# Performance work log

Hardware: AMD Instinct MI355X
Metric: run time of the kernel (lower is better)

Reference implementation:

```python
import jax, jax.numpy as jnp
import numpy as np

H = 768
NH = 12
HD = H // NH


def setup_inputs() -> dict:
    key = jax.random.key(0)
    ks = jax.random.split(key, 12)
    B, S = 2, 2048
    s = 1.0 / np.sqrt(H)
    inp = {
        "hidden_states": jax.random.normal(ks[0], (B, S, H), dtype=jnp.float32),
        "attention_mask": jnp.ones((B, S), dtype=jnp.float32),
        "Wq": jax.random.normal(ks[1], (H, H), dtype=jnp.float32) * s,
        "bq": jnp.zeros((H,), dtype=jnp.float32),
        "Wk": jax.random.normal(ks[2], (H, H), dtype=jnp.float32) * s,
        "bk": jnp.zeros((H,), dtype=jnp.float32),
        "Wv": jax.random.normal(ks[3], (H, H), dtype=jnp.float32) * s,
        "bv": jnp.zeros((H,), dtype=jnp.float32),
        "Wo": jax.random.normal(ks[4], (H, H), dtype=jnp.float32) * s,
        "bo": jnp.zeros((H,), dtype=jnp.float32),
        "ln_gamma": jnp.ones((H,), dtype=jnp.float32),
        "ln_beta": jnp.zeros((H,), dtype=jnp.float32),
    }
    return inp


def _split_heads(x):
    # [B,S,H] -> [B,NH,S,HD]
    B, S, _ = x.shape
    return x.reshape(B, S, NH, HD).transpose(0, 2, 1, 3)


def reference(hidden_states, attention_mask, Wq, bq, Wk, bk, Wv, bv, Wo, bo, ln_gamma, ln_beta):
    x = hidden_states
    q = _split_heads(x @ Wq.T + bq)
    k = _split_heads(x @ Wk.T + bk)
    v = _split_heads(x @ Wv.T + bv)
    # scores: [B,NH,S,S]
    scores = jnp.einsum("bhqd,bhkd->bhqk", q, k) / jnp.sqrt(jnp.float32(HD))
    mask = (1.0 - attention_mask)[:, None, None, :] * -10000.0
    scores = scores + mask
    probs = jax.nn.softmax(scores, axis=-1)  # dropout is identity at inference
    ctx = jnp.einsum("bhqk,bhkd->bhqd", probs, v)
    B, _, S, _ = ctx.shape
    ctx = ctx.transpose(0, 2, 1, 3).reshape(B, S, H)
    out = ctx @ Wo.T + bo
    y = out + x
    mu = jnp.mean(y, axis=-1, keepdims=True)
    var = jnp.var(y, axis=-1, keepdims=True)
    y = (y - mu) / jnp.sqrt(var + 1e-5)
    return y * ln_gamma + ln_beta
```

## Files before the change

kernel.cpp:

```cpp
#include <hip/hip_runtime.h>
#include <math.h>

#define HH 768
#define NHEADS 12
#define HDIM 64
#define SEQ 2048
#define NB 2
#define L2E 1.44269504088896f

typedef __attribute__((ext_vector_type(8))) short s8v;
typedef __attribute__((ext_vector_type(4))) short s4v;
typedef __attribute__((ext_vector_type(4))) float f4v;

static __device__ inline short f2bf(float f) {
    union { float f; unsigned u; } v; v.f = f;
    unsigned r = v.u + 0x7fff + ((v.u >> 16) & 1);
    return (short)(r >> 16);
}

#if __has_builtin(__builtin_amdgcn_exp2f)
#define EXP2(x) __builtin_amdgcn_exp2f(x)
#else
#define EXP2(x) __expf((x) * 0.6931471805599453f)
#endif

__device__ __forceinline__ unsigned cvt_pk_bf16(float a, float b) {
    unsigned r;
    asm("v_cvt_pk_bf16_f32 %0, %1, %2" : "=v"(r) : "v"(a), "v"(b));
    return r;
}

__device__ __forceinline__ void gld16(const void* g, void* l) {
    __builtin_amdgcn_global_load_lds(
        (const __attribute__((address_space(1))) void*)g,
        (__attribute__((address_space(3))) void*)l, 16, 0, 0);
}

__device__ __forceinline__ int kperm(int k) {
    return (k & ~31) | (((k >> 2) & 3) << 3) | (((k >> 4) & 1) << 2) | (k & 3);
}

#define XV8   393216
#define WV8   73728
__global__ __launch_bounds__(256)
void cvt_kernel(const float* __restrict__ X, short* __restrict__ Xb,
                const float* __restrict__ W0, short* __restrict__ W0b,
                const float* __restrict__ W1, short* __restrict__ W1b,
                const float* __restrict__ W2, short* __restrict__ W2b,
                const float* __restrict__ W3, short* __restrict__ W3b)
{
    int gid = blockIdx.x * 256 + threadIdx.x;
    const float* src; short* dst; size_t off;
    if      (gid < XV8)            { src = X;  dst = Xb;  off = gid; }
    else if (gid < XV8 + WV8)      { src = W0; dst = W0b; off = gid - XV8; }
    else if (gid < XV8 + 2*WV8)    { src = W1; dst = W1b; off = gid - XV8 - WV8; }
    else if (gid < XV8 + 3*WV8)    { src = W2; dst = W2b; off = gid - XV8 - 2*WV8; }
    else if (gid < XV8 + 4*WV8)    { src = W3; dst = W3b; off = gid - XV8 - 3*WV8; }
    else return;
    off *= 8;
    float4 a = *(const float4*)(src + off);
    float4 b = *(const float4*)(src + off + 4);
    s8v o;
    o[0] = f2bf(a.x); o[1] = f2bf(a.y); o[2] = f2bf(a.z); o[3] = f2bf(a.w);
    o[4] = f2bf(b.x); o[5] = f2bf(b.y); o[6] = f2bf(b.z); o[7] = f2bf(b.w);
    *(s8v*)(dst + off) = o;
}

#define NKT (HH/32)
template<int EPI>
__global__ __launch_bounds__(256)
void gemm_mfma(const short* __restrict__ A,
               const short* __restrict__ Wq, const short* __restrict__ Wk,
               const short* __restrict__ Wv,
               const float* __restrict__ bq, const float* __restrict__ bk,
               const float* __restrict__ bv,
               short* __restrict__ Qo, short* __restrict__ Ko, short* __restrict__ Vo,
               const float* __restrict__ Xres, float* __restrict__ Fo)
{
    __shared__ __align__(16) short As[2*64*32];
    __shared__ __align__(16) short Bs[2*128*32];

    const int tid  = threadIdx.x;
    const int w    = tid >> 6;
    const int lane = tid & 63;
    const int g    = lane >> 4;
    const int r    = lane & 15;
    const int wr   = w >> 1;
    const int wc   = w & 1;

    const int NI   = (EPI == 0) ? 4 : 2;
    const int BBUF = (EPI == 0) ? 4096 : 2048;

    const int NBX = (EPI == 0) ? 18 : 12;
    const int NXB = (EPI == 0) ? 144 : 96;
    const int wg  = (blockIdx.x & 7) * NXB + (blockIdx.x >> 3);
    const int bx  = wg % NBX;
    const int by  = wg / NBX;
    const int m0  = by * 64;

    int n0;
    int seg = 0;
    const short* Wb; const float* bias; short* outp; float scale;
    if (EPI == 0) {
        seg = bx / 6;
        n0 = (bx % 6) * 128;
        Wb   = seg == 0 ? Wq : seg == 1 ? Wk : Wv;
        bias = seg == 0 ? bq : seg == 1 ? bk : bv;
        outp = seg == 0 ? Qo : seg == 1 ? Ko : Vo;
        scale = seg == 0 ? (0.125f * L2E) : 1.0f;
    } else {
        n0 = bx * 64;
        Wb = Wq; bias = bq; outp = nullptr; scale = 1.0f;
    }

    const int uline = tid >> 3;
    const int us    = tid & 7;
    const int srow  = 2*uline + (us >> 2);
    const int scol  = 8 * ((us & 3) ^ (uline & 3));
    const short* Asrc  = A  + (size_t)(m0 + srow) * HH + scol;
    const short* Bsrc0 = Wb + (size_t)(n0 + srow) * HH + scol;
    const short* Bsrc1 = (EPI == 0) ? (Wb + (size_t)(n0 + 64 + srow) * HH + scol) : nullptr;

    #define GSTAGE(KT, DB) do { const int k0 = (KT) * 32;                      \
        gld16(Asrc  + k0, As + (DB)*2048 + w*512);                             \
        gld16(Bsrc0 + k0, Bs + (DB)*BBUF + w*512);                             \
        if (EPI == 0) gld16(Bsrc1 + k0, Bs + (DB)*BBUF + 2048 + w*512);        \
    } while (0)

    f4v acc[2][4];
    #pragma unroll
    for (int i = 0; i < 2; i++)
        #pragma unroll
        for (int j = 0; j < 4; j++) acc[i][j] = (f4v){0.f,0.f,0.f,0.f};

    const int keyg  = (g ^ ((r >> 1) & 3)) * 8;
    const int abase = (wr*16 + (r >> 1))*64 + (r & 1)*32 + keyg;
    const int wcl   = (EPI == 0) ? wc*32 : wc*16;
    const int bbase = (wcl + (r >> 1))*64 + (r & 1)*32 + keyg;

    #define GCOMPUTE(DB) do {                                                  \
        const short* Ab = As + (DB)*2048;                                      \
        const short* Bb = Bs + (DB)*BBUF;                                      \
        s8v af[2], bf[4];                                                      \
        _Pragma("unroll")                                                      \
        for (int mi = 0; mi < 2; mi++)                                         \
            af[mi] = *(const s8v*)(Ab + abase + mi*512);                       \
        _Pragma("unroll")                                                      \
        for (int ni = 0; ni < NI; ni++)                                        \
            bf[ni] = *(const s8v*)(Bb + bbase + ni*512);                       \
        __builtin_amdgcn_s_setprio(1);                                         \
        _Pragma("unroll")                                                      \
        for (int mi = 0; mi < 2; mi++)                                         \
            _Pragma("unroll")                                                  \
            for (int ni = 0; ni < NI; ni++)                                    \
                acc[mi][ni] = __builtin_amdgcn_mfma_f32_16x16x32_bf16(         \
                    af[mi], bf[ni], acc[mi][ni], 0, 0, 0);                     \
        __builtin_amdgcn_s_setprio(0);                                         \
    } while (0)

    GSTAGE(0, 0);

    for (int kt = 0; kt < NKT; ++kt) {
        if (kt + 1 < NKT) {
            GSTAGE(kt + 1, (kt + 1) & 1);
            if constexpr (EPI == 0) asm volatile("s_waitcnt vmcnt(3)" ::: "memory");
            else                    asm volatile("s_waitcnt vmcnt(2)" ::: "memory");
        } else {
            asm volatile("s_waitcnt vmcnt(0)" ::: "memory");
        }
        __builtin_amdgcn_s_barrier();
        GCOMPUTE(kt & 1);
        __builtin_amdgcn_s_barrier();
    }

    if (EPI == 0) {
        if (seg < 2) {
            #pragma unroll
            for (int mi = 0; mi < 2; mi++) {
                #pragma unroll
                for (int j = 0; j < 4; j++) {
                    const int m = m0 + wr*32 + mi*16 + 4*g + j;
                    const int bb = m >> 11;
                    const int s  = m & 2047;
                    #pragma unroll
                    for (int ni = 0; ni < 4; ni++) {
                        const int n = n0 + wc*64 + ni*16 + r;
                        const int h = n >> 6;
                        const int d = n & 63;
                        outp[((size_t)((bb*NHEADS + h)*SEQ) + s)*HDIM + d] =
                            f2bf((acc[mi][ni][j] + bias[n]) * scale);
                    }
                }
            }
        } else {
            #pragma unroll
            for (int mi = 0; mi < 2; mi++) {
                const int m  = m0 + wr*32 + mi*16 + 4*g;
                const int bb = m >> 11;
                const int s  = m & 2047;
                const int sp = kperm(s);
                #pragma unroll
                for (int ni = 0; ni < 4; ni++) {
                    const int n = n0 + wc*64 + ni*16 + r;
                    const int h = n >> 6;
                    const int d = n & 63;
                    s4v pk;
                    #pragma unroll
                    for (int j = 0; j < 4; j++)
                        pk[j] = f2bf(acc[mi][ni][j] + bias[n]);
                    *(s4v*)(outp + ((size_t)((bb*NHEADS + h)*HDIM) + d)*SEQ + sp) = pk;
                }
            }
        }
    } else {
        #pragma unroll
        for (int mi = 0; mi < 2; mi++) {
            #pragma unroll
            for (int j = 0; j < 4; j++) {
                const int m = m0 + wr*32 + mi*16 + 4*g + j;
                #pragma unroll
                for (int ni = 0; ni < 2; ni++) {
                    const int n = n0 + wc*32 + ni*16 + r;
                    Fo[(size_t)m*HH + n] = acc[mi][ni][j] + bias[n] + Xres[(size_t)m*HH + n];
                }
            }
        }
    }
    #undef GSTAGE
    #undef GCOMPUTE
}

#define NPAIR (SEQ/64)
__global__ __launch_bounds__(512, 4)
void attn_mfma(const short* __restrict__ Q, const short* __restrict__ K,
               const short* __restrict__ VT, const float* __restrict__ mask,
               short* __restrict__ CTX)
{
    const int wgid = (blockIdx.x & 7) * 96 + (blockIdx.x >> 3);
    const int qt = wgid & 31;
    const int bh = wgid >> 5;
    const int h  = bh % NHEADS;
    const int b  = bh / NHEADS;

    const size_t hb = (size_t)(b * NHEADS + h);
    const short* Qg  = Q  + hb * SEQ * HDIM;
    const short* Kg  = K  + hb * SEQ * HDIM;
    const short* VTg = VT + hb * HDIM * SEQ;

    __shared__ __align__(16) char lds[40960];
    char* Kbase = lds;
    char* Vbase = lds + 16384;
    float* Mf   = (float*)(lds + 32768);

    const int tid  = threadIdx.x;
    const int w    = tid >> 6;
    const int grp  = w >> 2;
    const int wq   = w & 3;
    const int lane = tid & 63;
    const int g    = lane >> 4;
    const int r    = lane & 15;
    const int q0   = qt * 64;

    const short* qrow = Qg + (size_t)(q0 + wq*16 + r) * HDIM;
    const s8v qf0 = *(const s8v*)(qrow + 8*g);
    const s8v qf1 = *(const s8v*)(qrow + 8*g + 32);

    {
        float4 mv = *(const float4*)(mask + b*SEQ + tid*4);
        f4v md;
        md[0] = (mv.x - 1.0f) * (10000.0f * L2E);
        md[1] = (mv.y - 1.0f) * (10000.0f * L2E);
        md[2] = (mv.z - 1.0f) * (10000.0f * L2E);
        md[3] = (mv.w - 1.0f) * (10000.0f * L2E);
        *(f4v*)(Mf + kperm(tid*4)) = md;
    }

    f4v acc[4];
    #pragma unroll
    for (int t = 0; t < 4; t++) acc[t] = (f4v){0.f, 0.f, 0.f, 0.f};
    f4v accl = (f4v){0.f, 0.f, 0.f, 0.f};
    const s8v ones = (s8v){0x3F80, 0x3F80, 0x3F80, 0x3F80,
                           0x3F80, 0x3F80, 0x3F80, 0x3F80};

    const int srow = lane >> 3;
    const int scol = 8 * ((lane & 7) ^ srow);

    #define STAGE(PT, DB) do {                                                 \
        const int pk0 = (PT) * 64;                                             \
        char* kd = Kbase + (DB)*8192 + w*1024;                                 \
        gld16(Kg + (size_t)(pk0 + 8*w + srow)*HDIM + scol, kd);                \
        char* vd = Vbase + (DB)*8192 + w*1024;                                 \
        gld16(VTg + (size_t)(8*w + srow)*SEQ + pk0 + scol, vd);                \
    } while (0)

    STAGE(0, 0);
    __syncthreads();

    for (int pt = 0; pt < NPAIR; ++pt) {
        const int db = pt & 1;
        if (pt + 1 < NPAIR) {
            STAGE(pt + 1, db ^ 1);
            asm volatile("s_waitcnt vmcnt(2)" ::: "memory");
        } else {
            asm volatile("s_waitcnt vmcnt(0)" ::: "memory");
        }
        __builtin_amdgcn_s_barrier();

        const char* Kc = Kbase + db*8192 + grp*4096;
        const char* Vc = Vbase + db*8192;

        const float* mrow = Mf + pt*64 + grp*32 + 8*g;
        f4v z0 = *(const f4v*)(mrow);
        f4v z1 = *(const f4v*)(mrow + 4);

        __builtin_amdgcn_s_setprio(1);
        {
            const int sw = (r & 7) << 4;
            const char* kb0 = Kc + r * 128;
            const char* kb1 = Kc + (16 + r) * 128;
            s8v ka0 = *(const s8v*)(kb0 + ((16*g)      ^ sw));
            s8v ka1 = *(const s8v*)(kb0 + ((16*g + 64) ^ sw));
            s8v kc0 = *(const s8v*)(kb1 + ((16*g)      ^ sw));
            s8v kc1 = *(const s8v*)(kb1 + ((16*g + 64) ^ sw));
            z0 = __builtin_amdgcn_mfma_f32_16x16x32_bf16(ka0, qf0, z0, 0, 0, 0);
            z0 = __builtin_amdgcn_mfma_f32_16x16x32_bf16(ka1, qf1, z0, 0, 0, 0);
            z1 = __builtin_amdgcn_mfma_f32_16x16x32_bf16(kc0, qf0, z1, 0, 0, 0);
            z1 = __builtin_amdgcn_mfma_f32_16x16x32_bf16(kc1, qf1, z1, 0, 0, 0);
        }
        __builtin_amdgcn_s_setprio(0);

        #pragma unroll
        for (int i = 0; i < 4; i++) {
            z0[i] = EXP2(z0[i]);
            z1[i] = EXP2(z1[i]);
        }

        union { unsigned u[4]; s8v v; } pfu;
        pfu.u[0] = cvt_pk_bf16(z0[0], z0[1]);
        pfu.u[1] = cvt_pk_bf16(z0[2], z0[3]);
        pfu.u[2] = cvt_pk_bf16(z1[0], z1[1]);
        pfu.u[3] = cvt_pk_bf16(z1[2], z1[3]);
        const s8v pf = pfu.v;

        accl = __builtin_amdgcn_mfma_f32_16x16x32_bf16(pf, ones, accl, 0, 0, 0);

        __builtin_amdgcn_s_setprio(1);
        #pragma unroll
        for (int t4 = 0; t4 < 4; t4++) {
            const int vrow = 16*t4 + r;
            s8v vf = *(const s8v*)(Vc + vrow*128 + ((16*(4*grp + g)) ^ ((r & 7) << 4)));
            acc[t4] = __builtin_amdgcn_mfma_f32_16x16x32_bf16(pf, vf, acc[t4], 0, 0, 0);
        }
        __builtin_amdgcn_s_setprio(0);

        __builtin_amdgcn_s_barrier();
    }

    __syncthreads();
    if (grp == 1) {
        float* mb = (float*)(lds + wq*5120 + lane*80);
        *(f4v*)(mb)      = acc[0];
        *(f4v*)(mb + 4)  = acc[1];
        *(f4v*)(mb + 8)  = acc[2];
        *(f4v*)(mb + 12) = acc[3];
        *(f4v*)(mb + 16) = accl;
    }
    __syncthreads();
    if (grp == 0) {
        const float* mb = (const float*)(lds + wq*5120 + lane*80);
        acc[0] += *(const f4v*)(mb);
        acc[1] += *(const f4v*)(mb + 4);
        acc[2] += *(const f4v*)(mb + 8);
        acc[3] += *(const f4v*)(mb + 12);
        accl   += *(const f4v*)(mb + 16);

        #pragma unroll
        for (int i = 0; i < 4; i++) {
            const float invl = 1.0f / accl[i];
            const size_t rowbase = ((size_t)(b*SEQ) + q0 + wq*16 + 4*g + i) * HH + h*HDIM;
            #pragma unroll
            for (int t4 = 0; t4 < 4; t4++)
                CTX[rowbase + 16*t4 + r] = f2bf(acc[t4][i] * invl);
        }
    }
    #undef STAGE
}

__global__ __launch_bounds__(256)
void ln_kernel(float* __restrict__ y, const float* __restrict__ gamma,
               const float* __restrict__ beta)
{
    const int row = blockIdx.x;
    float* p = y + (size_t)row * HH;
    const int tid = threadIdx.x;

    float v[3];
    float s = 0.f, ss = 0.f;
    #pragma unroll
    for (int i = 0; i < 3; i++) {
        float x = p[tid + i*256];
        v[i] = x;
        s += x;
        ss += x * x;
    }
    #pragma unroll
    for (int off = 32; off > 0; off >>= 1) {
        s  += __shfl_down(s,  off);
        ss += __shfl_down(ss, off);
    }
    __shared__ float sbuf[4], ssbuf[4];
    __shared__ float mu_s, rstd_s;
    const int wave = tid >> 6;
    if ((tid & 63) == 0) { sbuf[wave] = s; ssbuf[wave] = ss; }
    __syncthreads();
    if (tid == 0) {
        float S  = sbuf[0] + sbuf[1] + sbuf[2] + sbuf[3];
        float SS = ssbuf[0] + ssbuf[1] + ssbuf[2] + ssbuf[3];
        float mu = S * (1.0f / HH);
        float var = SS * (1.0f / HH) - mu * mu;
        mu_s = mu;
        rstd_s = rsqrtf(var + 1e-5f);
    }
    __syncthreads();
    const float mu = mu_s, rstd = rstd_s;
    #pragma unroll
    for (int i = 0; i < 3; i++) {
        const int c = tid + i*256;
        p[c] = (v[i] - mu) * rstd * gamma[c] + beta[c];
    }
}

extern "C" void kernel_launch(void* const* d_in, const int* in_sizes, int n_in,
                              void* d_out, int out_size, void* d_ws, size_t ws_size,
                              hipStream_t stream)
{
    const float* x     = (const float*)d_in[0];
    const float* mask  = (const float*)d_in[1];
    const float* Wq    = (const float*)d_in[2];
    const float* bq    = (const float*)d_in[3];
    const float* Wk    = (const float*)d_in[4];
    const float* bk    = (const float*)d_in[5];
    const float* Wv    = (const float*)d_in[6];
    const float* bv    = (const float*)d_in[7];
    const float* Wo    = (const float*)d_in[8];
    const float* bo    = (const float*)d_in[9];
    const float* gamma = (const float*)d_in[10];
    const float* beta  = (const float*)d_in[11];

    const size_t PER = (size_t)NB * NHEADS * SEQ * HDIM;
    const size_t WSZ = (size_t)HH * HH;
    short* wsS  = (short*)d_ws;
    short* Xb   = wsS;
    short* Wqb  = wsS + PER;
    short* Wkb  = Wqb + WSZ;
    short* Wvb  = Wkb + WSZ;
    short* Wob  = Wvb + WSZ;
    short* Qb   = Wob + WSZ;
    short* Kb   = Qb + PER;
    short* VTb  = Kb + PER;
    short* CTXb = Xb;
    float* out  = (float*)d_out;

    cvt_kernel<<<2688, 256, 0, stream>>>(x, Xb, Wq, Wqb, Wk, Wkb, Wv, Wvb, Wo, Wob);

    gemm_mfma<0><<<1152, 256, 0, stream>>>(
        Xb, Wqb, Wkb, Wvb, bq, bk, bv, Qb, Kb, VTb, nullptr, nullptr);

    attn_mfma<<<768, 512, 0, stream>>>(Qb, Kb, VTb, mask, CTXb);

    gemm_mfma<1><<<768, 256, 0, stream>>>(
        CTXb, Wob, nullptr, nullptr, bo, nullptr, nullptr,
        nullptr, nullptr, nullptr, x, out);

    ln_kernel<<<NB*SEQ, 256, 0, stream>>>(out, gamma, beta);
}
```

Before: 101.4 us.

## Fuse fp32-to-bf16 conversion into GEMM tile loads, drop separate convert kernel

Removes the standalone conversion kernel. The GEMMs now stream fp32 X and weight tiles into LDS with a swizzled layout and convert them to bf16 fragments with packed cvt instructions when reading LDS. This saves one launch and a full write and re-read of bf16 copies. In exchange, global and LDS traffic per tile doubles (fp32), LDS use grows, and conversion ALU work is repeated across every block that reads the same tile.

```diff
diff --git a/kernel.cpp b/kernel.cpp
--- a/kernel.cpp
+++ b/kernel.cpp
@@ -40,45 +40,31 @@
     return (k & ~31) | (((k >> 2) & 3) << 3) | (((k >> 4) & 1) << 2) | (k & 3);
 }
 
-#define XV8   393216
-#define WV8   73728
-__global__ __launch_bounds__(256)
-void cvt_kernel(const float* __restrict__ X, short* __restrict__ Xb,
-                const float* __restrict__ W0, short* __restrict__ W0b,
-                const float* __restrict__ W1, short* __restrict__ W1b,
-                const float* __restrict__ W2, short* __restrict__ W2b,
-                const float* __restrict__ W3, short* __restrict__ W3b)
-{
-    int gid = blockIdx.x * 256 + threadIdx.x;
-    const float* src; short* dst; size_t off;
-    if      (gid < XV8)            { src = X;  dst = Xb;  off = gid; }
-    else if (gid < XV8 + WV8)      { src = W0; dst = W0b; off = gid - XV8; }
-    else if (gid < XV8 + 2*WV8)    { src = W1; dst = W1b; off = gid - XV8 - WV8; }
-    else if (gid < XV8 + 3*WV8)    { src = W2; dst = W2b; off = gid - XV8 - 2*WV8; }
-    else if (gid < XV8 + 4*WV8)    { src = W3; dst = W3b; off = gid - XV8 - 3*WV8; }
-    else return;
-    off *= 8;
-    float4 a = *(const float4*)(src + off);
-    float4 b = *(const float4*)(src + off + 4);
-    s8v o;
-    o[0] = f2bf(a.x); o[1] = f2bf(a.y); o[2] = f2bf(a.z); o[3] = f2bf(a.w);
-    o[4] = f2bf(b.x); o[5] = f2bf(b.y); o[6] = f2bf(b.z); o[7] = f2bf(b.w);
-    *(s8v*)(dst + off) = o;
+__device__ __forceinline__ s8v frag_from_f32(const float* rowbase, int R, int g) {
+    const int gr = (g ^ (R & 3)) * 8;
+    const int sw = ((R >> 2) & 1) * 4;
+    f4v lo = *(const f4v*)(rowbase + gr + sw);
+    f4v hi = *(const f4v*)(rowbase + gr + (sw ^ 4));
+    union { unsigned u[4]; s8v v; } o;
+    o.u[0] = cvt_pk_bf16(lo[0], lo[1]);
+    o.u[1] = cvt_pk_bf16(lo[2], lo[3]);
+    o.u[2] = cvt_pk_bf16(hi[0], hi[1]);
+    o.u[3] = cvt_pk_bf16(hi[2], hi[3]);
+    return o.v;
 }
 
 #define NKT (HH/32)
 template<int EPI>
 __global__ __launch_bounds__(256)
-void gemm_mfma(const short* __restrict__ A,
-               const short* __restrict__ Wq, const short* __restrict__ Wk,
-               const short* __restrict__ Wv,
+void gemm_mfma(const void* __restrict__ Av,
+               const float* __restrict__ Wq, const float* __restrict__ Wk,
+               const float* __restrict__ Wv,
                const float* __restrict__ bq, const float* __restrict__ bk,
                const float* __restrict__ bv,
                short* __restrict__ Qo, short* __restrict__ Ko, short* __restrict__ Vo,
                const float* __restrict__ Xres, float* __restrict__ Fo)
 {
-    __shared__ __align__(16) short As[2*64*32];
-    __shared__ __align__(16) short Bs[2*128*32];
+    __shared__ __align__(16) char lds[(EPI == 0) ? 49152 : 24576];
 
     const int tid  = threadIdx.x;
     const int w    = tid >> 6;
@@ -88,8 +74,7 @@
     const int wr   = w >> 1;
     const int wc   = w & 1;
 
-    const int NI   = (EPI == 0) ? 4 : 2;
-    const int BBUF = (EPI == 0) ? 4096 : 2048;
+    const int NI = (EPI == 0) ? 4 : 2;
 
     const int NBX = (EPI == 0) ? 18 : 12;
     const int NXB = (EPI == 0) ? 144 : 96;
@@ -100,7 +85,7 @@
 
     int n0;
     int seg = 0;
-    const short* Wb; const float* bias; short* outp; float scale;
+    const float* Wb; const float* bias; short* outp; float scale;
     if (EPI == 0) {
         seg = bx / 6;
         n0 = (bx % 6) * 128;
@@ -113,18 +98,54 @@
         Wb = Wq; bias = bq; outp = nullptr; scale = 1.0f;
     }
 
-    const int uline = tid >> 3;
-    const int us    = tid & 7;
-    const int srow  = 2*uline + (us >> 2);
-    const int scol  = 8 * ((us & 3) ^ (uline & 3));
-    const short* Asrc  = A  + (size_t)(m0 + srow) * HH + scol;
-    const short* Bsrc0 = Wb + (size_t)(n0 + srow) * HH + scol;
-    const short* Bsrc1 = (EPI == 0) ? (Wb + (size_t)(n0 + 64 + srow) * HH + scol) : nullptr;
+    #define F32COL(ROW, U) ((((U) >> 1) ^ ((ROW) & 3)) * 8 + (((U) & 1) ^ (((ROW) >> 2) & 1)) * 4)
+
+    const float* AsrcF[2];
+    const short* AsrcH = nullptr;
+    const float* BsrcF[4];
+
+    if (EPI == 0) {
+        const float* X = (const float*)Av;
+        #pragma unroll
+        for (int k = 0; k < 2; k++) {
+            const int s = tid + k*256, row = s >> 3, u = s & 7;
+            AsrcF[k] = X + (size_t)(m0 + row) * HH + F32COL(row, u);
+        }
+        #pragma unroll
+        for (int k = 0; k < 4; k++) {
+            const int s = tid + k*256, row = s >> 3, u = s & 7;
+            BsrcF[k] = Wb + (size_t)(n0 + row) * HH + F32COL(row, u);
+        }
+    } else {
+        const short* Ah = (const short*)Av;
+        const int uline = tid >> 3, us = tid & 7;
+        AsrcH = Ah + (size_t)(m0 + 2*uline + (us >> 2)) * HH + 8*((us & 3) ^ (uline & 3));
+        #pragma unroll
+        for (int k = 0; k < 2; k++) {
+            const int s = tid + k*256, row = s >> 3, u = s & 7;
+            BsrcF[k] = Wb + (size_t)(n0 + row) * HH + F32COL(row, u);
+        }
+    }
+
+    float* AF = (float*)lds;
+    short* AH = (short*)lds;
+    float* BF = (float*)(lds + ((EPI == 0) ? 16384 : 8192));
+    const int BSTR = (EPI == 0) ? 4096 : 2048;
 
     #define GSTAGE(KT, DB) do { const int k0 = (KT) * 32;                      \
-        gld16(Asrc  + k0, As + (DB)*2048 + w*512);                             \
-        gld16(Bsrc0 + k0, Bs + (DB)*BBUF + w*512);                             \
-        if (EPI == 0) gld16(Bsrc1 + k0, Bs + (DB)*BBUF + 2048 + w*512);        \
+        if (EPI == 0) {                                                        \
+            _Pragma("unroll")                                                  \
+            for (int k = 0; k < 2; k++)                                        \
+                gld16(AsrcF[k] + k0, AF + (DB)*2048 + k*1024 + w*256);         \
+            _Pragma("unroll")                                                  \
+            for (int k = 0; k < 4; k++)                                        \
+                gld16(BsrcF[k] + k0, BF + (DB)*4096 + k*1024 + w*256);         \
+        } else {                                                               \
+            gld16(AsrcH + k0, AH + (DB)*2048 + w*512);                         \
+            _Pragma("unroll")                                                  \
+            for (int k = 0; k < 2; k++)                                        \
+                gld16(BsrcF[k] + k0, BF + (DB)*2048 + k*1024 + w*256);         \
+        }                                                                      \
     } while (0)
 
     f4v acc[2][4];
@@ -134,20 +155,31 @@
         for (int j = 0; j < 4; j++) acc[i][j] = (f4v){0.f,0.f,0.f,0.f};
 
     const int keyg  = (g ^ ((r >> 1) & 3)) * 8;
-    const int abase = (wr*16 + (r >> 1))*64 + (r & 1)*32 + keyg;
-    const int wcl   = (EPI == 0) ? wc*32 : wc*16;
-    const int bbase = (wcl + (r >> 1))*64 + (r & 1)*32 + keyg;
+    const int abaseH = (wr*16 + (r >> 1))*64 + (r & 1)*32 + keyg;
 
     #define GCOMPUTE(DB) do {                                                  \
-        const short* Ab = As + (DB)*2048;                                      \
-        const short* Bb = Bs + (DB)*BBUF;                                      \
         s8v af[2], bf[4];                                                      \
-        _Pragma("unroll")                                                      \
-        for (int mi = 0; mi < 2; mi++)                                         \
-            af[mi] = *(const s8v*)(Ab + abase + mi*512);                       \
-        _Pragma("unroll")                                                      \
-        for (int ni = 0; ni < NI; ni++)                                        \
-            bf[ni] = *(const s8v*)(Bb + bbase + ni*512);                       \
+        if (EPI == 0) {                                                        \
+            const float* Ab = AF + (DB)*2048;                                  \
+            _Pragma("unroll")                                                  \
+            for (int mi = 0; mi < 2; mi++) {                                   \
+                const int R = wr*32 + mi*16 + r;                               \
+                af[mi] = frag_from_f32(Ab + R*32, R, g);                       \
+            }                                                                  \
+        } else {                                                               \
+            const short* Ab = AH + (DB)*2048;                                  \
+            _Pragma("unroll")                                                  \
+            for (int mi = 0; mi < 2; mi++)                                     \
+                af[mi] = *(const s8v*)(Ab + abaseH + mi*512);                  \
+        }                                                                      \
+        {                                                                      \
+            const float* Bb = BF + (DB)*BSTR;                                  \
+            _Pragma("unroll")                                                  \
+            for (int ni = 0; ni < NI; ni++) {                                  \
+                const int R = ((EPI == 0) ? wc*64 : wc*32) + ni*16 + r;        \
+                bf[ni] = frag_from_f32(Bb + R*32, R, g);                       \
+            }                                                                  \
+        }                                                                      \
         __builtin_amdgcn_s_setprio(1);                                         \
         _Pragma("unroll")                                                      \
         for (int mi = 0; mi < 2; mi++)                                         \
@@ -163,8 +195,8 @@
     for (int kt = 0; kt < NKT; ++kt) {
         if (kt + 1 < NKT) {
             GSTAGE(kt + 1, (kt + 1) & 1);
-            if constexpr (EPI == 0) asm volatile("s_waitcnt vmcnt(3)" ::: "memory");
-            else                    asm volatile("s_waitcnt vmcnt(2)" ::: "memory");
+            if constexpr (EPI == 0) asm volatile("s_waitcnt vmcnt(6)" ::: "memory");
+            else                    asm volatile("s_waitcnt vmcnt(3)" ::: "memory");
         } else {
             asm volatile("s_waitcnt vmcnt(0)" ::: "memory");
         }
@@ -228,6 +260,7 @@
     }
     #undef GSTAGE
     #undef GCOMPUTE
+    #undef F32COL
 }
 
 #define NPAIR (SEQ/64)
@@ -448,28 +481,20 @@
     const float* beta  = (const float*)d_in[11];
 
     const size_t PER = (size_t)NB * NHEADS * SEQ * HDIM;
-    const size_t WSZ = (size_t)HH * HH;
     short* wsS  = (short*)d_ws;
-    short* Xb   = wsS;
-    short* Wqb  = wsS + PER;
-    short* Wkb  = Wqb + WSZ;
-    short* Wvb  = Wkb + WSZ;
-    short* Wob  = Wvb + WSZ;
-    short* Qb   = Wob + WSZ;
+    short* Qb   = wsS;
     short* Kb   = Qb + PER;
     short* VTb  = Kb + PER;
-    short* CTXb = Xb;
+    short* CTXb = VTb + PER;
     float* out  = (float*)d_out;
 
-    cvt_kernel<<<2688, 256, 0, stream>>>(x, Xb, Wq, Wqb, Wk, Wkb, Wv, Wvb, Wo, Wob);
-
     gemm_mfma<0><<<1152, 256, 0, stream>>>(
-        Xb, Wqb, Wkb, Wvb, bq, bk, bv, Qb, Kb, VTb, nullptr, nullptr);
+        x, Wq, Wk, Wv, bq, bk, bv, Qb, Kb, VTb, nullptr, nullptr);
 
     attn_mfma<<<768, 512, 0, stream>>>(Qb, Kb, VTb, mask, CTXb);
 
     gemm_mfma<1><<<768, 256, 0, stream>>>(
-        CTXb, Wob, nullptr, nullptr, bo, nullptr, nullptr,
+        CTXb, Wo, nullptr, nullptr, bo, nullptr, nullptr,
         nullptr, nullptr, nullptr, x, out);
 
     ln_kernel<<<NB*SEQ, 256, 0, stream>>>(out, gamma, beta);
```

Result: no change. 101.1 us (-0.3%).
